# Kernel optimization log

Measured on AMD Instinct MI355X. Metric: run time of the kernel, lower is better.

The kernel has to match this reference:

```python
import jax, jax.numpy as jnp
import numpy as np
from jax import lax

KS = 21      # ksize
SCALE = 4    # downscale stride


def _conv(x, w, b=None, padding='SAME'):
    # x: NCHW, w: OIHW
    y = lax.conv_general_dilated(x, w, (1, 1), padding,
                                 dimension_numbers=('NCHW', 'OIHW', 'NCHW'))
    if b is not None:
        y = y + b[None, :, None, None]
    return y


def _deg_kernel_net(z, conv0_w, conv0_b, res_w1, res_b1, res_w2, res_b2, last_w, last_b):
    # conv3x3 -> nb EDSR ResBlocks (conv-relu-conv + residual) -> conv1x1 to ksize^2
    h = _conv(z, conv0_w, conv0_b)
    for i in range(res_w1.shape[0]):  # fixed small layer count
        r = _conv(jax.nn.relu(_conv(h, res_w1[i], res_b1[i])), res_w2[i], res_b2[i])
        h = h + r
    return _conv(h, last_w, last_b)  # (B, ksize^2, H', W')


def setup_inputs() -> dict:
    key = jax.random.key(0)
    ks = jax.random.split(key, 10)
    B, C, H, W = 8, 3, 256, 256
    nf, nb, k2 = 64, 8, KS * KS
    s = 0.05  # keep activations tame through 8 residual blocks
    return {
        'x': jax.random.normal(ks[0], (B, C, H, W), jnp.float32),
        'z': jax.random.normal(ks[1], (B, C, H // SCALE, W // SCALE), jnp.float32),
        'conv0_w': jax.random.normal(ks[2], (nf, C, 3, 3), jnp.float32) * s,
        'conv0_b': jax.random.normal(ks[3], (nf,), jnp.float32) * s,
        'res_w1': jax.random.normal(ks[4], (nb, nf, nf, 3, 3), jnp.float32) * s,
        'res_b1': jax.random.normal(ks[5], (nb, nf), jnp.float32) * s,
        'res_w2': jax.random.normal(ks[6], (nb, nf, nf, 3, 3), jnp.float32) * s,
        'res_b2': jax.random.normal(ks[7], (nb, nf), jnp.float32) * s,
        'last_w': jax.random.normal(ks[8], (k2, nf, 1, 1), jnp.float32) * s,
        'last_b': jax.random.normal(ks[9], (k2,), jnp.float32) * s,
    }


def reference(x, z, conv0_w, conv0_b, res_w1, res_b1, res_w2, res_b2, last_w, last_b):
    B, C, H, W = x.shape
    hz, wz = z.shape[2], z.shape[3]
    k2 = KS * KS

    # spatially-varying kernel, normalized over the ksize^2 taps
    kernel = _deg_kernel_net(z, conv0_w, conv0_b, res_w1, res_b1,
                             res_w2, res_b2, last_w, last_b)
    kernel = kernel.reshape(B, 1, k2, hz, wz)
    kernel = kernel / (kernel.sum(axis=2, keepdims=True) + 1e-8)

    # reflection pad then unfold (im2col) with stride = scale
    p = KS // 2
    xp = jnp.pad(x.reshape(B * C, 1, H, W), ((0, 0), (0, 0), (p, p), (p, p)),
                 mode='reflect')
    patches = lax.conv_general_dilated_patches(
        xp, (KS, KS), (SCALE, SCALE), 'VALID',
        dimension_numbers=('NCHW', 'OIHW', 'NCHW'))  # (B*C, k2, hz, wz)
    patches = patches.reshape(B, C, k2, hz, wz)

    out = (patches * kernel).sum(axis=2)  # (B, C, hz, wz)
    return out, kernel.reshape(B, k2, hz, wz)
```

## Files before the change

### kernel.cpp

```cpp
#include <hip/hip_runtime.h>


#define NB 8
#define NF 64
#define SP 4096
#define PS 66
#define PS2 4356
#define K2 441
#define K2P 448
#define RES_WSTRIDE (64*64*9)
#define WF_RES 36864
#define WF_C0  1792
#define WTA_N  28672

typedef double vdbl4 __attribute__((ext_vector_type(4)));

#define T_AI 0
#define T_AK 64
#define T_BK 128
#define T_BJ 192
#define T_DI 256
#define T_DJ 512

__global__ void probe_mfma(double* __restrict__ probe)
{
    int l = threadIdx.x;
    vdbl4 z = {0.0, 0.0, 0.0, 0.0};
    vdbl4 r1 = __builtin_amdgcn_mfma_f64_16x16x4f64((double)l, 1.0, z, 0, 0, 0);
    vdbl4 r2 = __builtin_amdgcn_mfma_f64_16x16x4f64(1.0, (double)l, z, 0, 0, 0);
#pragma unroll
    for (int r = 0; r < 4; ++r) {
        probe[r * 64 + l]       = r1[r];
        probe[256 + r * 64 + l] = r2[r];
    }
}

__global__ void decode_probe(const double* __restrict__ probe, int* __restrict__ tabs)
{
    int t = threadIdx.x;
    const double* d1 = probe;
    const double* d2 = probe + 256;
    bool fA = ((((int)d1[0]) & 3) == 0);
    bool fB = ((((int)d2[0]) & 3) == 0);
    int v1 = (int)d1[t], v2 = (int)d2[t];
    tabs[T_DI + t] = fA ? (v1 - 96) >> 2 : (v1 - 6) >> 4;
    tabs[T_DJ + t] = fB ? (v2 - 96) >> 2 : (v2 - 6) >> 4;
    if (t < 64) {
        tabs[T_AI + t] = fA ? (t & 15) : (t >> 2);
        tabs[T_AK + t] = fA ? (t >> 4) : (t & 3);
        tabs[T_BK + t] = fB ? (t >> 4) : (t & 3);
        tabs[T_BJ + t] = fB ? (t & 15) : (t >> 2);
    }
}

__global__ void prep_zpad(const float* __restrict__ z, double* __restrict__ zp)
{
    int i = blockIdx.x * blockDim.x + threadIdx.x;
    if (i >= NB * 3 * SP) return;
    int bc = i >> 12, p = i & 4095, y = p >> 6, x = p & 63;
    zp[(size_t)(bc * PS + y + 1) * PS + x + 1] = (double)z[i];
}

__global__ void prep_convw_frag(const float* __restrict__ src, double* __restrict__ dst,
                                const int* __restrict__ tabs,
                                int CIN, int nlayer, int wstride)
{
    int i = blockIdx.x * blockDim.x + threadIdx.x;
    int NS = (CIN * 9 + 3) / 4;
    int M  = NS * 256;
    if (i >= nlayer * M) return;
    int li  = i / M;
    int rem = i - li * M;
    int t   = rem >> 8;
    int j   = rem & 255;
    int mt  = j >> 6;
    int l   = j & 63;
    int kg  = t * 4 + tabs[T_AK + l];
    int oc  = mt * 16 + tabs[T_AI + l];
    int c   = kg / 9;
    int tap = kg - c * 9;
    dst[i] = (kg < CIN * 9) ? (double)src[li * wstride + (oc * CIN + c) * 9 + tap] : 0.0;
}

__global__ void prep_bias_frag(const float* __restrict__ src, double* __restrict__ dst,
                               const int* __restrict__ tabs, int nlayer)
{
    int i = blockIdx.x * blockDim.x + threadIdx.x;
    if (i >= nlayer * 1024) return;
    int li  = i >> 10;
    int j   = i & 1023;
    int mtr = j >> 6;
    int l   = j & 63;
    int mt  = mtr >> 2, r = mtr & 3;
    dst[i] = (double)src[li * 64 + mt * 16 + tabs[T_DI + r * 64 + l]];
}

__global__ void prep_lastwa(const float* __restrict__ lw, const float* __restrict__ lb,
                            const int* __restrict__ tabs,
                            double* __restrict__ wta, double* __restrict__ lbp)
{
    int i = blockIdx.x * blockDim.x + threadIdx.x;
    if (i < WTA_N) {
        int kk = i / (28 * 64);
        int rem = i - kk * (28 * 64);
        int mt = rem >> 6;
        int l  = rem & 63;
        int c  = kk * 4 + tabs[T_AK + l];
        int T  = mt * 16 + tabs[T_AI + l];
        wta[i] = (T < K2) ? (double)lw[T * 64 + c] : 0.0;
    }
    if (i < K2P) lbp[i] = (i < K2) ? (double)lb[i] : 0.0;
}

__global__ void prep_wsum(const float* __restrict__ lw, const float* __restrict__ lb,
                          double* __restrict__ wsum)
{
    int c = threadIdx.x;
    if (c < 64) {
        double s = 0.0;
        for (int t = 0; t < K2; ++t) s += (double)lw[t * 64 + c];
        wsum[c] = s;
    }
    if (c == 64) {
        double s = 0.0;
        for (int t = 0; t < K2; ++t) s += (double)lb[t];
        wsum[64] = s;
    }
}

template<int CIN, bool RELU, bool RESADD>
__global__ __launch_bounds__(256, 2)
void conv3x3_mfma(const double* __restrict__ in, const double* __restrict__ WF,
                  const double* __restrict__ BF, const int* __restrict__ tabs,
                  const double* __restrict__ res, double* __restrict__ out)
{
    constexpr int KT = CIN * 9;
    constexpr int NS = (KT + 3) / 4;
    constexpr int G  = (NS + 8) / 9;

    const int bid = blockIdx.x;
    const int b   = bid & 7;
    const int y0  = bid >> 3;
    const int tid = threadIdx.x;
    const int w   = tid >> 6;
    const int l   = tid & 63;
    const int mi  = w >> 1, ni = w & 1;
    const int mt0 = mi * 2, nt0 = ni * 2;

    const int kB = tabs[T_BK + l];
    const int jB = tabs[T_BJ + l];

    int offp[9];
#pragma unroll
    for (int s = 0; s < 9; ++s) {
        int kg  = s * 4 + kB;
        int off = 0;
        if (KT >= 36 || kg < KT) {
            int c   = kg / 9;
            int tap = kg - c * 9;
            int dy  = tap / 3, dx = tap - dy * 3;
            off = c * PS2 + dy * PS + dx;
        }
        offp[s] = off + jB + nt0 * 16;
    }

    const double* bbase = in + (size_t)b * CIN * PS2 + (size_t)y0 * PS;

    vdbl4 acc[2][2];
#pragma unroll
    for (int mt = 0; mt < 2; ++mt)
#pragma unroll
        for (int r = 0; r < 4; ++r) {
            double bv = BF[((mt0 + mt) * 4 + r) * 64 + l];
            acc[mt][0][r] = bv;
            acc[mt][1][r] = bv;
        }

    double aS[3][2], bS[3][2];
    auto ldA = [&](int t, int slot) {
        const double* p = WF + (size_t)t * 256 + l;
        aS[slot][0] = p[mt0 * 64];
        aS[slot][1] = p[(mt0 + 1) * 64];
    };
    auto ldB = [&](size_t cg, int s, int slot) {
        const double* p = bbase + cg + offp[s];
        bS[slot][0] = p[0];
        bS[slot][1] = p[16];
    };
    auto step = [&](int slot) {
        acc[0][0] = __builtin_amdgcn_mfma_f64_16x16x4f64(aS[slot][0], bS[slot][0], acc[0][0], 0, 0, 0);
        acc[0][1] = __builtin_amdgcn_mfma_f64_16x16x4f64(aS[slot][0], bS[slot][1], acc[0][1], 0, 0, 0);
        acc[1][0] = __builtin_amdgcn_mfma_f64_16x16x4f64(aS[slot][1], bS[slot][0], acc[1][0], 0, 0, 0);
        acc[1][1] = __builtin_amdgcn_mfma_f64_16x16x4f64(aS[slot][1], bS[slot][1], acc[1][1], 0, 0, 0);
    };

    ldA(0, 0); ldB(0, 0, 0);
    ldA(1, 1); ldB(0, 1, 1);

    for (int g = 0; g < G; ++g) {
        const size_t cg = (size_t)g * 4 * PS2;
#pragma unroll
        for (int s = 0; s < 9; ++s) {
            const int t = g * 9 + s;
            if (KT % 36 != 0 && t >= NS) break;
            const int tp = t + 2;
            if (tp < NS) {
                const int    ps  = (s + 2 < 9) ? s + 2 : s - 7;
                const size_t pcg = (s + 2 < 9) ? cg : cg + 4 * PS2;
                ldA(tp, (s + 2) % 3);
                ldB(pcg, ps, (s + 2) % 3);
            }
            step(s % 3);
        }
    }

    int iD[4], jD[4];
#pragma unroll
    for (int r = 0; r < 4; ++r) {
        iD[r] = tabs[T_DI + r * 64 + l];
        jD[r] = tabs[T_DJ + r * 64 + l];
    }
#pragma unroll
    for (int mt = 0; mt < 2; ++mt)
#pragma unroll
        for (int nt = 0; nt < 2; ++nt)
#pragma unroll
            for (int r = 0; r < 4; ++r) {
                int oc = (mt0 + mt) * 16 + iD[r];
                int x  = (nt0 + nt) * 16 + jD[r];
                size_t idx = (size_t)(b * NF + oc) * PS2 + (size_t)(y0 + 1) * PS + x + 1;
                double val = acc[mt][nt][r];
                if (RELU)   val = fmax(val, 0.0);
                if (RESADD) val += res[idx];
                out[idx] = val;
            }
}

__global__ __launch_bounds__(256, 2)
void lastconv_mfma(const double* __restrict__ hp, const double* __restrict__ wta,
                   const double* __restrict__ lbp, const int* __restrict__ tabs,
                   const double* __restrict__ inv_sums, float* __restrict__ kraw)
{
    const int bid = blockIdx.x;
    const int b   = bid / 224;
    const int rem = bid - b * 224;
    const int tg  = rem >> 5;
    const int pc  = rem & 31;
    const int tid = threadIdx.x;
    const int w   = tid >> 6;
    const int l   = tid & 63;
    const int mt  = tg * 4 + w;

    const int kB = tabs[T_BK + l];
    const int jB = tabs[T_BJ + l];
    int iD[4], jD[4];
#pragma unroll
    for (int r = 0; r < 4; ++r) {
        iD[r] = tabs[T_DI + r * 64 + l];
        jD[r] = tabs[T_DJ + r * 64 + l];
    }

    double avs[16];
#pragma unroll
    for (int kk = 0; kk < 16; ++kk)
        avs[kk] = wta[((size_t)kk * 28 + mt) * 64 + l];

    double bias[4];
#pragma unroll
    for (int r = 0; r < 4; ++r)
        bias[r] = lbp[mt * 16 + iD[r]];

    const double* hb = hp + (size_t)b * NF * PS2;
    float* kb = kraw + (size_t)b * K2 * SP;

    for (int q = 0; q < 2; ++q) {
        const int P0  = pc * 128 + q * 64;
        const int row = P0 >> 6;
        const double* hrow = hb + (size_t)(row + 1) * PS + 1 + jB;

        const double* isrow = inv_sums + (size_t)b * SP + P0;
        double isv[4][4];
#pragma unroll
        for (int j = 0; j < 4; ++j)
#pragma unroll
            for (int r = 0; r < 4; ++r)
                isv[j][r] = isrow[j * 16 + jD[r]];

        vdbl4 acc[4];
#pragma unroll
        for (int j = 0; j < 4; ++j)
#pragma unroll
            for (int r = 0; r < 4; ++r)
                acc[j][r] = bias[r];

        double bc[4], bn[4], bn2[4];
#pragma unroll
        for (int j = 0; j < 4; ++j)
            bc[j] = hrow[(size_t)kB * PS2 + j * 16];
#pragma unroll
        for (int j = 0; j < 4; ++j)
            bn[j] = hrow[(size_t)(4 + kB) * PS2 + j * 16];

        for (int kk = 0; kk < 16; ++kk) {
            if (kk < 14) {
                const double* np = hrow + (size_t)((kk + 2) * 4 + kB) * PS2;
#pragma unroll
                for (int j = 0; j < 4; ++j) bn2[j] = np[j * 16];
            }
#pragma unroll
            for (int j = 0; j < 4; ++j)
                acc[j] = __builtin_amdgcn_mfma_f64_16x16x4f64(avs[kk], bc[j], acc[j], 0, 0, 0);
#pragma unroll
            for (int j = 0; j < 4; ++j) { bc[j] = bn[j]; bn[j] = bn2[j]; }
        }

#pragma unroll
        for (int r = 0; r < 4; ++r) {
            int T = mt * 16 + iD[r];
            if (T < K2) {
                float* p = kb + (size_t)T * SP + P0;
                p[jD[r]]      = (float)(acc[0][r] * isv[0][r]);
                p[16 + jD[r]] = (float)(acc[1][r] * isv[1][r]);
                p[32 + jD[r]] = (float)(acc[2][r] * isv[2][r]);
                p[48 + jD[r]] = (float)(acc[3][r] * isv[3][r]);
            }
        }
    }
}

__global__ __launch_bounds__(256)
void sums_kernel(const double* __restrict__ hp, const double* __restrict__ wsum,
                 double* __restrict__ inv_sums)
{
    int i = blockIdx.x * 256 + threadIdx.x;
    int b = i >> 12, p = i & 4095;
    int y = p >> 6, x = p & 63;
    const double* hb = hp + (size_t)b * NF * PS2 + (size_t)(y + 1) * PS + 1 + x;
    double s = wsum[64];
    for (int c = 0; c < 64; ++c) s += hb[(size_t)c * PS2] * wsum[c];
    inv_sums[b * SP + p] = 1.0 / (s + 1e-8);
}

__global__ __launch_bounds__(256)
void apply_kernel(const float* __restrict__ x, const float* __restrict__ kout,
                  float* __restrict__ out)
{
    const int bid   = blockIdx.x;
    const int b     = bid >> 6;
    const int row   = bid & 63;
    const int tid   = threadIdx.x;
    const int chunk = tid >> 6;
    const int px    = tid & 63;
    const int p     = row * 64 + px;

    const float* xb = x + (size_t)b * 3 * 65536;
    const float* kb = kout + (size_t)b * K2 * SP + p;

    auto xaddr = [&](int tt) -> const float* {
        int ty = tt / 21, tx = tt - ty * 21;
        int gr = row * 4 + ty - 10;
        int gc = px * 4 + tx - 10;
        gr = gr < 0 ? -gr : (gr > 255 ? 510 - gr : gr);
        gc = gc < 0 ? -gc : (gc > 255 ? 510 - gc : gc);
        return xb + gr * 256 + gc;
    };

    float o0 = 0.f, o1 = 0.f, o2 = 0.f;
    const int t0 = chunk * 111;
    const int t1 = (t0 + 111 < K2) ? t0 + 111 : K2;

    int t = t0;
    for (; t + 4 <= t1; t += 4) {
        float kn0 = kb[(size_t)(t    ) * SP];
        float kn1 = kb[(size_t)(t + 1) * SP];
        float kn2 = kb[(size_t)(t + 2) * SP];
        float kn3 = kb[(size_t)(t + 3) * SP];
        const float* x0 = xaddr(t);
        const float* x1 = xaddr(t + 1);
        const float* x2 = xaddr(t + 2);
        const float* x3 = xaddr(t + 3);
        o0 = fmaf(x0[0], kn0, o0); o1 = fmaf(x0[65536], kn0, o1); o2 = fmaf(x0[131072], kn0, o2);
        o0 = fmaf(x1[0], kn1, o0); o1 = fmaf(x1[65536], kn1, o1); o2 = fmaf(x1[131072], kn1, o2);
        o0 = fmaf(x2[0], kn2, o0); o1 = fmaf(x2[65536], kn2, o1); o2 = fmaf(x2[131072], kn2, o2);
        o0 = fmaf(x3[0], kn3, o0); o1 = fmaf(x3[65536], kn3, o1); o2 = fmaf(x3[131072], kn3, o2);
    }
    for (; t < t1; ++t) {
        float kn = kb[(size_t)t * SP];
        const float* xp = xaddr(t);
        o0 = fmaf(xp[0],      kn, o0);
        o1 = fmaf(xp[65536],  kn, o1);
        o2 = fmaf(xp[131072], kn, o2);
    }

    __shared__ float red[3][4][64];
    if (chunk > 0) {
        red[0][chunk][px] = o0;
        red[1][chunk][px] = o1;
        red[2][chunk][px] = o2;
    }
    __syncthreads();
    if (chunk == 0) {
        o0 += red[0][1][px] + red[0][2][px] + red[0][3][px];
        o1 += red[1][1][px] + red[1][2][px] + red[1][3][px];
        o2 += red[2][1][px] + red[2][2][px] + red[2][3][px];
        out[(b * 3 + 0) * SP + p] = o0;
        out[(b * 3 + 1) * SP + p] = o1;
        out[(b * 3 + 2) * SP + p] = o2;
    }
}

extern "C" void kernel_launch(void* const* d_in, const int* in_sizes, int n_in,
                              void* d_out, int out_size, void* d_ws, size_t ws_size,
                              hipStream_t stream)
{
    (void)in_sizes; (void)n_in; (void)out_size; (void)ws_size;

    const float* x = (const float*)d_in[0];
    const float* z = (const float*)d_in[1];

    float* out  = (float*)d_out;
    float* kout = (float*)d_out + NB * 3 * SP;

    double* wd    = (double*)d_ws;
    double* probe = wd;
    int*    tabs  = (int*)(wd + 512);
    double* wf0   = wd + 1024;
    double* wf1   = wf0 + WF_C0;
    double* wf2   = wf1 + 8 * WF_RES;
    double* bf0   = wf2 + 8 * WF_RES;
    double* bf1   = bf0 + 1024;
    double* bf2   = bf1 + 8 * 1024;
    double* wta   = bf2 + 8 * 1024;
    double* lbp   = wta + WTA_N;
    double* wsum  = lbp + K2P;
    double* zp    = wsum + 72;
    double* hp    = zp + NB * 3 * PS2;
    double* tp    = hp + NB * NF * PS2;
    double* sums  = tp;

    hipMemsetAsync(zp, 0, (size_t)NB * 3 * PS2 * sizeof(double), stream);
    hipMemsetAsync(hp, 0, (size_t)NB * NF * PS2 * sizeof(double), stream);
    hipMemsetAsync(tp, 0, (size_t)NB * NF * PS2 * sizeof(double), stream);

    probe_mfma<<<1, 64, 0, stream>>>(probe);
    decode_probe<<<1, 256, 0, stream>>>(probe, tabs);

    prep_zpad<<<(NB * 3 * SP + 255) / 256, 256, 0, stream>>>(z, zp);
    prep_convw_frag<<<(WF_C0 + 255) / 256, 256, 0, stream>>>(
        (const float*)d_in[2], wf0, tabs, 3, 1, 0);
    prep_convw_frag<<<(8 * WF_RES + 255) / 256, 256, 0, stream>>>(
        (const float*)d_in[4], wf1, tabs, 64, 8, RES_WSTRIDE);
    prep_convw_frag<<<(8 * WF_RES + 255) / 256, 256, 0, stream>>>(
        (const float*)d_in[6], wf2, tabs, 64, 8, RES_WSTRIDE);
    prep_bias_frag<<<(1024 + 255) / 256, 256, 0, stream>>>(
        (const float*)d_in[3], bf0, tabs, 1);
    prep_bias_frag<<<(8 * 1024 + 255) / 256, 256, 0, stream>>>(
        (const float*)d_in[5], bf1, tabs, 8);
    prep_bias_frag<<<(8 * 1024 + 255) / 256, 256, 0, stream>>>(
        (const float*)d_in[7], bf2, tabs, 8);
    prep_lastwa<<<(WTA_N + 255) / 256, 256, 0, stream>>>(
        (const float*)d_in[8], (const float*)d_in[9], tabs, wta, lbp);
    prep_wsum<<<1, 128, 0, stream>>>(
        (const float*)d_in[8], (const float*)d_in[9], wsum);

    conv3x3_mfma<3,  false, false><<<512, 256, 0, stream>>>(zp, wf0, bf0, tabs, nullptr, hp);
    for (int i = 0; i < 8; ++i) {
        conv3x3_mfma<64, true,  false><<<512, 256, 0, stream>>>(
            hp, wf1 + i * WF_RES, bf1 + i * 1024, tabs, nullptr, tp);
        conv3x3_mfma<64, false, true ><<<512, 256, 0, stream>>>(
            tp, wf2 + i * WF_RES, bf2 + i * 1024, tabs, hp, hp);
    }
    sums_kernel<<<128, 256, 0, stream>>>(hp, wsum, sums);
    lastconv_mfma<<<1792, 256, 0, stream>>>(hp, wta, lbp, tabs, sums, kout);
    apply_kernel<<<512, 256, 0, stream>>>(x, kout, out);
}
```

Baseline: 891.4 us.

## Stage conv input rows in double-buffered LDS for 64-channel 3x3 convs

For the residual convs (input channels a multiple of 4), each block now cooperatively loads a 4-channel by 3-row by 66-column slab of the padded input into shared memory. The slab is double-buffered: the next group's global loads are issued before the MFMA steps and written to LDS afterwards. MFMA B operands are then read from LDS instead of making repeated scattered global loads per lane. The cost is an added __syncthreads per channel group and extra LDS use; the conv0 path keeps the old direct-load code.

```diff
diff --git a/kernel.cpp b/kernel.cpp
--- a/kernel.cpp
+++ b/kernel.cpp
@@ -12,6 +12,7 @@
 #define WF_RES 36864
 #define WF_C0  1792
 #define WTA_N  28672
+#define SBN 792
 
 typedef double vdbl4 __attribute__((ext_vector_type(4)));
 
@@ -150,19 +151,7 @@
     const int kB = tabs[T_BK + l];
     const int jB = tabs[T_BJ + l];
 
-    int offp[9];
-#pragma unroll
-    for (int s = 0; s < 9; ++s) {
-        int kg  = s * 4 + kB;
-        int off = 0;
-        if (KT >= 36 || kg < KT) {
-            int c   = kg / 9;
-            int tap = kg - c * 9;
-            int dy  = tap / 3, dx = tap - dy * 3;
-            off = c * PS2 + dy * PS + dx;
-        }
-        offp[s] = off + jB + nt0 * 16;
-    }
+    __shared__ double sB[2][SBN];
 
     const double* bbase = in + (size_t)b * CIN * PS2 + (size_t)y0 * PS;
 
@@ -181,11 +170,6 @@
         const double* p = WF + (size_t)t * 256 + l;
         aS[slot][0] = p[mt0 * 64];
         aS[slot][1] = p[(mt0 + 1) * 64];
-    };
-    auto ldB = [&](size_t cg, int s, int slot) {
-        const double* p = bbase + cg + offp[s];
-        bS[slot][0] = p[0];
-        bS[slot][1] = p[16];
     };
     auto step = [&](int slot) {
         acc[0][0] = __builtin_amdgcn_mfma_f64_16x16x4f64(aS[slot][0], bS[slot][0], acc[0][0], 0, 0, 0);
@@ -194,23 +178,119 @@
         acc[1][1] = __builtin_amdgcn_mfma_f64_16x16x4f64(aS[slot][1], bS[slot][1], acc[1][1], 0, 0, 0);
     };
 
-    ldA(0, 0); ldB(0, 0, 0);
-    ldA(1, 1); ldB(0, 1, 1);
-
-    for (int g = 0; g < G; ++g) {
-        const size_t cg = (size_t)g * 4 * PS2;
+    if constexpr (KT % 36 == 0) {
+        int offp[9];
 #pragma unroll
         for (int s = 0; s < 9; ++s) {
-            const int t = g * 9 + s;
-            if (KT % 36 != 0 && t >= NS) break;
-            const int tp = t + 2;
-            if (tp < NS) {
-                const int    ps  = (s + 2 < 9) ? s + 2 : s - 7;
-                const size_t pcg = (s + 2 < 9) ? cg : cg + 4 * PS2;
-                ldA(tp, (s + 2) % 3);
-                ldB(pcg, ps, (s + 2) % 3);
-            }
-            step(s % 3);
+            int kg  = s * 4 + kB;
+            int c   = kg / 9;
+            int tap = kg - c * 9;
+            int dy  = tap / 3, dx = tap - dy * 3;
+            offp[s] = c * 198 + dy * 66 + dx + jB + nt0 * 16;
+        }
+        int cS[4], roS[4], coS[4];
+#pragma unroll
+        for (int k = 0; k < 4; ++k) {
+            int e  = tid + k * 256;
+            int c  = e / 198;
+            int rm = e - c * 198;
+            cS[k]  = c;
+            roS[k] = rm / 66;
+            coS[k] = rm - roS[k] * 66;
+        }
+        auto ldBl = [&](const double* sbuf, int s, int slot) {
+            bS[slot][0] = sbuf[offp[s]];
+            bS[slot][1] = sbuf[offp[s] + 16];
+        };
+
+        {
+            double r[4];
+#pragma unroll
+            for (int k = 0; k < 4; ++k) {
+                int e = tid + k * 256;
+                if (e < SBN)
+                    r[k] = bbase[(size_t)cS[k] * PS2 + roS[k] * PS + coS[k]];
+            }
+#pragma unroll
+            for (int k = 0; k < 4; ++k) {
+                int e = tid + k * 256;
+                if (e < SBN) sB[0][e] = r[k];
+            }
+        }
+        __syncthreads();
+        ldA(0, 0);
+        ldA(1, 1);
+
+        for (int g = 0; g < G; ++g) {
+            const double* cbuf = sB[g & 1];
+            double r[4];
+            if (g + 1 < G) {
+                const double* gsrc = bbase + (size_t)(g + 1) * 4 * PS2;
+#pragma unroll
+                for (int k = 0; k < 4; ++k) {
+                    int e = tid + k * 256;
+                    if (e < SBN)
+                        r[k] = gsrc[(size_t)cS[k] * PS2 + roS[k] * PS + coS[k]];
+                }
+            }
+            ldBl(cbuf, 0, 0);
+            ldBl(cbuf, 1, 1);
+#pragma unroll
+            for (int s = 0; s < 9; ++s) {
+                const int t  = g * 9 + s;
+                const int tp = t + 2;
+                if (tp < NS) ldA(tp, (s + 2) % 3);
+                if (s + 2 <= 8) ldBl(cbuf, s + 2, (s + 2) % 3);
+                step(s % 3);
+            }
+            if (g + 1 < G) {
+                double* nbuf = sB[(g + 1) & 1];
+#pragma unroll
+                for (int k = 0; k < 4; ++k) {
+                    int e = tid + k * 256;
+                    if (e < SBN) nbuf[e] = r[k];
+                }
+            }
+            __syncthreads();
+        }
+    } else {
+        int offp[9];
+#pragma unroll
+        for (int s = 0; s < 9; ++s) {
+            int kg  = s * 4 + kB;
+            int off = 0;
+            if (kg < KT) {
+                int c   = kg / 9;
+                int tap = kg - c * 9;
+                int dy  = tap / 3, dx = tap - dy * 3;
+                off = c * PS2 + dy * PS + dx;
+            }
+            offp[s] = off + jB + nt0 * 16;
+        }
+        auto ldB = [&](size_t cg, int s, int slot) {
+            const double* p = bbase + cg + offp[s];
+            bS[slot][0] = p[0];
+            bS[slot][1] = p[16];
+        };
+
+        ldA(0, 0); ldB(0, 0, 0);
+        ldA(1, 1); ldB(0, 1, 1);
+
+        for (int g = 0; g < G; ++g) {
+            const size_t cg = (size_t)g * 4 * PS2;
+#pragma unroll
+            for (int s = 0; s < 9; ++s) {
+                const int t = g * 9 + s;
+                if (t >= NS) break;
+                const int tp = t + 2;
+                if (tp < NS) {
+                    const int    ps  = (s + 2 < 9) ? s + 2 : s - 7;
+                    const size_t pcg = (s + 2 < 9) ? cg : cg + 4 * PS2;
+                    ldA(tp, (s + 2) % 3);
+                    ldB(pcg, ps, (s + 2) % 3);
+                }
+                step(s % 3);
+            }
         }
     }
 
```

New measurement: 935.2 us. 4.9% more time.
